# Kernel tuning notes

Measured on AMD Instinct MI355X. Metric: run time of the kernel, lower is better.

Reference implementation:

```python
import jax, jax.numpy as jnp
import numpy as np
import math

B, S, H = 1, 2048, 2048
NH, NKV, HD = 32, 8, 64
GROUPS = NH // NKV
WINDOW = 128
ROPE_THETA = 150000.0
FACTOR = 32.0
ORIG_MAX = 4096.0
BETA_FAST = 32.0
BETA_SLOW = 1.0
SCALE = 1.0 / math.sqrt(HD)


def yarn_rope(q, k, position_ids):
    # q: [B,S,NH,HD], k: [B,S,NKV,HD]
    dim_half = HD // 2
    inv_freq = 1.0 / ROPE_THETA ** (jnp.arange(0, dim_half, 2, dtype=jnp.float32) / dim_half)
    wavelengths = 2.0 * jnp.pi / inv_freq
    ratio = ORIG_MAX / wavelengths
    alpha = jnp.clip((FACTOR * ratio - BETA_FAST) / (BETA_SLOW - BETA_FAST), 0.0, 1.0)
    inv_freq_scaled = inv_freq / FACTOR ** alpha
    freqs = position_ids[:, :, None].astype(jnp.float32) * inv_freq_scaled[None, None, :]
    freqs = jnp.repeat(freqs, 2, axis=-1)  # [B,S,dim_half]
    cos = jnp.cos(freqs)[:, :, None, :]
    sin = jnp.sin(freqs)[:, :, None, :]

    def rotate_half(x):
        # Faithful to source: x already has last dim == dim_half, so x2 is empty
        # and rotate_half(x) == x. Kept literal for exactness.
        x1 = x[..., :dim_half]
        x2 = x[..., dim_half:]
        return jnp.concatenate([-x2, x1], axis=-1)

    q_rot = q[..., :dim_half]
    k_rot = k[..., :dim_half]
    q_rot = q_rot * cos + rotate_half(q_rot) * sin
    k_rot = k_rot * cos + rotate_half(k_rot) * sin
    q = jnp.concatenate([q_rot, q[..., dim_half:]], axis=-1)
    k = jnp.concatenate([k_rot, k[..., dim_half:]], axis=-1)
    return q, k


def setup_inputs() -> dict:
    key = jax.random.key(0)
    ks = jax.random.split(key, 5)
    std = 0.02
    hidden_states = jax.random.normal(ks[0], (B, S, H), dtype=jnp.float32)
    position_ids = jnp.broadcast_to(jnp.arange(S, dtype=jnp.int32)[None, :], (B, S))
    Wq = jax.random.normal(ks[1], (H, NH * HD), dtype=jnp.float32) * std
    Wk = jax.random.normal(ks[2], (H, NKV * HD), dtype=jnp.float32) * std
    Wv = jax.random.normal(ks[3], (H, NKV * HD), dtype=jnp.float32) * std
    Wo = jax.random.normal(ks[4], (NH * HD, H), dtype=jnp.float32) * std
    return {"hidden_states": hidden_states, "position_ids": position_ids,
            "Wq": Wq, "Wk": Wk, "Wv": Wv, "Wo": Wo}


def reference(hidden_states, position_ids, Wq, Wk, Wv, Wo):
    q = (hidden_states @ Wq).reshape(B, S, NH, HD)
    k = (hidden_states @ Wk).reshape(B, S, NKV, HD)
    v = (hidden_states @ Wv).reshape(B, S, NKV, HD)
    q, k = yarn_rope(q, k, position_ids)
    # GQA: repeat kv heads to match query heads
    k = jnp.repeat(k, GROUPS, axis=2)  # [B,S,NH,HD]
    v = jnp.repeat(v, GROUPS, axis=2)
    # scores: [B,NH,S,S]
    scores = jnp.einsum('bqhd,bkhd->bhqk', q, k) * SCALE
    row = jnp.arange(S)[:, None]
    col = jnp.arange(S)[None, :]
    mask = ((jnp.abs(row - col) <= WINDOW) & (row >= col)).astype(jnp.float32)
    scores = scores + (1.0 - mask)[None, None, :, :] * -1e9
    attn = jax.nn.softmax(scores, axis=-1)
    out = jnp.einsum('bhqk,bkhd->bqhd', attn, v).reshape(B, S, NH * HD)
    return out @ Wo
```

## Files before the change

kernel.cpp:

```cpp
#include <hip/hip_runtime.h>

typedef unsigned short u16;
typedef short short8 __attribute__((ext_vector_type(8)));
typedef float f32x4 __attribute__((ext_vector_type(4)));

#define SLEN 2048
#define QKV_LD 3072
#define KOFF 2048
#define VOFF 2560

__device__ __forceinline__ u16 f2b(float f){
  unsigned u = __float_as_uint(f);
  u = u + 0x7FFFu + ((u >> 16) & 1u);
  return (u16)(u >> 16);
}
__device__ __forceinline__ float b2f(u16 v){
  unsigned u = ((unsigned)v) << 16;
  return __uint_as_float(u);
}

__device__ __forceinline__ void gload16(const u16* g, u16* l){
  __builtin_amdgcn_global_load_lds((const __attribute__((address_space(1))) void*)g,
                                   (__attribute__((address_space(3))) void*)l, 16, 0, 0);
}

__global__ __launch_bounds__(256) void k_prep(const float* __restrict__ hidden, u16* __restrict__ hb,
                                              const int* __restrict__ pos, float* __restrict__ g,
                                              const float* __restrict__ Wq, const float* __restrict__ Wk,
                                              const float* __restrict__ Wv, const float* __restrict__ Wo,
                                              u16* __restrict__ Wcat, u16* __restrict__ Wot){
  __shared__ float tile[64][68];
  int b = blockIdx.x, t = threadIdx.x;
  if (b < 4096){
    int i = b * 256 + t;
    float4 v = ((const float4*)hidden)[i];
    ushort4 o;
    o.x = f2b(v.x); o.y = f2b(v.y); o.z = f2b(v.z); o.w = f2b(v.w);
    ((ushort4*)hb)[i] = o;
    return;
  }
  if (b < 4224){
    int idx = (b - 4096) * 256 + t;
    int s = idx >> 4, i = idx & 15;
    float inv = 1.0f / powf(150000.0f, (float)i / 16.0f);
    float wl = 6.283185307179586f / inv;
    float ratio = 4096.0f / wl;
    float alpha = (32.0f * ratio - 32.0f) / (1.0f - 32.0f);
    alpha = fminf(fmaxf(alpha, 0.0f), 1.0f);
    float invs = inv / powf(32.0f, alpha);
    float th = (float)pos[s] * invs;
    double tt = (double)th;
    g[idx] = (float)(cos(tt) + sin(tt));
    return;
  }
  b -= 4224;
  const float* W; u16* D; int Nw, rowoff;
  if (b < 1024)      { W = Wq; D = Wcat; Nw = 2048; rowoff = 0; }
  else if (b < 1280) { W = Wk; D = Wcat; Nw = 512;  rowoff = 2048; b -= 1024; }
  else if (b < 1536) { W = Wv; D = Wcat; Nw = 512;  rowoff = 2560; b -= 1280; }
  else               { W = Wo; D = Wot;  Nw = 2048; rowoff = 0;    b -= 1536; }
  const int kt = b & 31, nt = b >> 5;
  const int k0 = kt * 64, n0 = nt * 64;
  #pragma unroll
  for (int i = 0; i < 4; ++i){
    int slot = i * 256 + t;
    int r = slot >> 4, c4 = (slot & 15) * 4;
    float4 v = *(const float4*)&W[(size_t)(k0 + r) * Nw + n0 + c4];
    tile[r][c4] = v.x; tile[r][c4+1] = v.y; tile[r][c4+2] = v.z; tile[r][c4+3] = v.w;
  }
  __syncthreads();
  #pragma unroll
  for (int i = 0; i < 4; ++i){
    int slot = i * 256 + t;
    int nl = slot >> 4, k4 = (slot & 15) * 4;
    ushort4 o;
    o.x = f2b(tile[k4][nl]);   o.y = f2b(tile[k4+1][nl]);
    o.z = f2b(tile[k4+2][nl]); o.w = f2b(tile[k4+3][nl]);
    *(ushort4*)&D[(size_t)(rowoff + n0 + nl) * 2048 + k0 + k4] = o;
  }
}

template<int OUTF32, int ROPE, int BM, int BN, int MINW>
__global__ __launch_bounds__(256, MINW) void k_gemm(const u16* __restrict__ A, const u16* __restrict__ Bt,
                                                    void* __restrict__ C, const float* __restrict__ g,
                                                    int M, int N, int K){
  constexpr int AG = BM / 32;
  constexpr int BG = BN / 32;
  constexpr int ASZ = BM * 64;
  constexpr int BSZ = BN * 64;
  constexpr int MR = BM / 32;
  constexpr int NR = BN / 32;
  __shared__ __align__(16) u16 Smem[2 * (ASZ + BSZ)];
  const int tid = threadIdx.x;
  const int lane = tid & 63;
  const int w = tid >> 6;
  const int wr = (w >> 1) * (BM / 2);
  const int wc = (w & 1) * (BN / 2);

  const int nbx = M / BM;
  const int nb  = nbx * (N / BN);
  const int q8  = nb >> 3;
  const int bo  = blockIdx.x;
  const int id2 = (bo & 7) * q8 + (bo >> 3);
  const int m0 = (id2 % nbx) * BM;
  const int n0 = (id2 / nbx) * BN;

  const int rl = lane >> 3;
  const int sc = ((lane & 7) ^ rl) << 3;
  const u16* Ag[AG]; const u16* Bg[BG];
  int Ad[AG], Bd[BG];
  #pragma unroll
  for (int i = 0; i < AG; ++i){
    int row0 = w * (AG * 8) + i * 8;
    Ag[i] = A + (size_t)(m0 + row0 + rl) * K + sc;
    Ad[i] = row0 * 64;
  }
  #pragma unroll
  for (int i = 0; i < BG; ++i){
    int row0 = w * (BG * 8) + i * 8;
    Bg[i] = Bt + (size_t)(n0 + row0 + rl) * K + sc;
    Bd[i] = 2 * ASZ + row0 * 64;
  }

  const int fr = lane & 15;
  const int g4 = lane >> 4;

  f32x4 acc[MR][NR] = {};

  auto stage = [&](int buf, int k0){
    #pragma unroll
    for (int i = 0; i < AG; ++i) gload16(Ag[i] + k0, Smem + Ad[i] + buf * ASZ);
    #pragma unroll
    for (int i = 0; i < BG; ++i) gload16(Bg[i] + k0, Smem + Bd[i] + buf * BSZ);
  };

  stage(0, 0);
  int buf = 0;
  const int nt = K >> 6;
  for (int kt = 0; kt < nt; ++kt){
    if (kt + 1 < nt){
      stage(buf ^ 1, (kt + 1) << 6);
      if constexpr (AG + BG == 6)      asm volatile("s_waitcnt vmcnt(6)" ::: "memory");
      else if constexpr (AG + BG == 7) asm volatile("s_waitcnt vmcnt(7)" ::: "memory");
      else                             asm volatile("s_waitcnt vmcnt(8)" ::: "memory");
    } else {
      asm volatile("s_waitcnt vmcnt(0)" ::: "memory");
    }
    __builtin_amdgcn_s_barrier();
    __builtin_amdgcn_sched_barrier(0);
    {
      const u16* Asb = Smem + buf * ASZ;
      const u16* Bsb = Smem + 2 * ASZ + buf * BSZ;
      #pragma unroll
      for (int kk = 0; kk < 2; ++kk){
        const int sw = (((kk * 4 + g4)) ^ (fr & 7)) << 3;
        short8 af[MR], bf[NR];
        #pragma unroll
        for (int m = 0; m < MR; ++m)
          af[m] = *(const short8*)&Asb[(wr + m * 16 + fr) * 64 + sw];
        #pragma unroll
        for (int j = 0; j < NR; ++j)
          bf[j] = *(const short8*)&Bsb[(wc + j * 16 + fr) * 64 + sw];
        #pragma unroll
        for (int m = 0; m < MR; ++m)
          #pragma unroll
          for (int j = 0; j < NR; ++j)
            acc[m][j] = __builtin_amdgcn_mfma_f32_16x16x32_bf16(af[m], bf[j], acc[m][j], 0, 0, 0);
      }
    }
    __builtin_amdgcn_sched_barrier(0);
    __builtin_amdgcn_s_barrier();
    buf ^= 1;
  }

  const int r4 = g4 * 4;
  #pragma unroll
  for (int m = 0; m < MR; ++m)
    #pragma unroll
    for (int j = 0; j < NR; ++j)
      #pragma unroll
      for (int v = 0; v < 4; ++v){
        size_t row = (size_t)(m0 + wr + m * 16 + r4 + v);
        size_t col = (size_t)(n0 + wc + j * 16 + fr);
        float x = acc[m][j][v];
        if (OUTF32){
          ((float*)C)[row * N + col] = x;
        } else {
          if (ROPE){
            int c = (int)col;
            int cj = c & 63;
            if (c < 2560 && cj < 32) x *= g[row * 16 + (cj >> 1)];
            if (c < 2048) x *= 0.125f;
          }
          ((u16*)C)[row * N + col] = f2b(x);
        }
      }
}

#define PST 168
__global__ __launch_bounds__(512, 4) void k_attn(const u16* __restrict__ qkv, u16* __restrict__ aout){
  __shared__ __align__(16) u16 Vt[64 * 264];
  __shared__ __align__(16) u16 P[8 * 16 * PST];
  const int tid = threadIdx.x;
  const int lane = tid & 63;
  const int w = tid >> 6;
  const int id = blockIdx.x;
  const int id2 = (id & 7) * 64 + (id >> 3);
  const int h = id2 >> 4;
  const int q0 = (id2 & 15) * 128;
  const int kvh = h >> 2;
  const int kv0 = q0 - 128;

  {
    const u16* Vg = qkv + VOFF + kvh * 64;
    #pragma unroll
    for (int i = 0; i < 4; ++i){
      int slot = i * 512 + tid;
      int kk = slot >> 3, d8 = (slot & 7) * 8;
      int ks = kv0 + kk; if (ks < 0) ks = 0;
      int ck = kk ^ ((d8 >> 4) << 3);
      short8 v = *(const short8*)(Vg + (size_t)ks * QKV_LD + d8);
      #pragma unroll
      for (int e = 0; e < 8; ++e) Vt[(d8 + e) * 264 + ck] = (u16)v[e];
    }
  }

  const int fr = lane & 15;
  const int kc8 = (lane >> 4) * 8;
  const int r4 = (lane >> 4) * 4;
  const int tt = w >> 2;
  const int wl = w & 3;
  const int nw0 = wl & ~1;
  const int c0 = nw0 * 16;
  const int qt = q0 + tt * 64;
  const int kbase = qt - 128;
  u16* Pw = P + w * 16 * PST;
  const u16* Qg = qkv + h * 64;
  const u16* Kg = qkv + KOFF + kvh * 64;

  short8 qa[2];
  {
    int qrow = qt + wl * 16 + fr;
    qa[0] = *(const short8*)(Qg + (size_t)qrow * QKV_LD + kc8);
    qa[1] = *(const short8*)(Qg + (size_t)qrow * QKV_LD + 32 + kc8);
  }

  f32x4 sc[10];
  __builtin_amdgcn_s_setprio(1);
  #pragma unroll
  for (int n = 0; n < 10; ++n){
    int kr = kbase + (nw0 + n) * 16 + fr;
    int krc = kr < 0 ? 0 : kr;
    short8 kb0 = *(const short8*)(Kg + (size_t)krc * QKV_LD + kc8);
    short8 kb1 = *(const short8*)(Kg + (size_t)krc * QKV_LD + 32 + kc8);
    f32x4 z = {0.f, 0.f, 0.f, 0.f};
    z = __builtin_amdgcn_mfma_f32_16x16x32_bf16(qa[0], kb0, z, 0, 0, 0);
    z = __builtin_amdgcn_mfma_f32_16x16x32_bf16(qa[1], kb1, z, 0, 0, 0);
    sc[n] = z;
  }
  __builtin_amdgcn_s_setprio(0);

  float inv_l[4];
  #pragma unroll
  for (int j = 0; j < 4; ++j){
    int q = qt + wl * 16 + r4 + j;
    float mx = -3.0e38f;
    #pragma unroll
    for (int n = 0; n < 10; ++n){
      int key = kbase + (nw0 + n) * 16 + fr;
      bool valid = (key >= 0) && (key <= q) && (key >= q - 128);
      float s = valid ? sc[n][j] : -1.0e30f;
      sc[n][j] = s;
      mx = fmaxf(mx, s);
    }
    mx = fmaxf(mx, __shfl_xor(mx, 1));
    mx = fmaxf(mx, __shfl_xor(mx, 2));
    mx = fmaxf(mx, __shfl_xor(mx, 4));
    mx = fmaxf(mx, __shfl_xor(mx, 8));
    float sum = 0.f;
    #pragma unroll
    for (int n = 0; n < 10; ++n){
      float pp = exp2f((sc[n][j] - mx) * 1.4426950408889634f);
      sc[n][j] = pp;
      sum += pp;
    }
    sum += __shfl_xor(sum, 1);
    sum += __shfl_xor(sum, 2);
    sum += __shfl_xor(sum, 4);
    sum += __shfl_xor(sum, 8);
    inv_l[j] = 1.0f / sum;
  }

  #pragma unroll
  for (int n = 0; n < 10; ++n)
    #pragma unroll
    for (int j = 0; j < 4; ++j)
      Pw[(r4 + j) * PST + n * 16 + fr] = f2b(sc[n][j]);

  asm volatile("s_waitcnt lgkmcnt(0)" ::: "memory");
  __syncthreads();

  f32x4 ov[4] = {};
  __builtin_amdgcn_s_setprio(1);
  #pragma unroll
  for (int kc = 0; kc < 5; ++kc){
    short8 pa = *(const short8*)&Pw[fr * PST + kc * 32 + kc8];
    #pragma unroll
    for (int f = 0; f < 4; ++f){
      short8 vb = *(const short8*)&Vt[(f * 16 + fr) * 264 + tt * 64 + c0 + kc * 32 + (kc8 ^ (f << 3))];
      ov[f] = __builtin_amdgcn_mfma_f32_16x16x32_bf16(pa, vb, ov[f], 0, 0, 0);
    }
  }
  __builtin_amdgcn_s_setprio(0);

  #pragma unroll
  for (int f = 0; f < 4; ++f)
    #pragma unroll
    for (int j = 0; j < 4; ++j){
      int q = qt + wl * 16 + r4 + j;
      int col = h * 64 + f * 16 + fr;
      aout[(size_t)q * 2048 + col] = f2b(ov[f][j] * inv_l[j]);
    }
}

extern "C" void kernel_launch(void* const* d_in, const int* in_sizes, int n_in,
                              void* d_out, int out_size, void* d_ws, size_t ws_size,
                              hipStream_t stream) {
  const float* hidden = (const float*)d_in[0];
  const int*   pos    = (const int*)d_in[1];
  const float* Wq     = (const float*)d_in[2];
  const float* Wk     = (const float*)d_in[3];
  const float* Wv     = (const float*)d_in[4];
  const float* Wo     = (const float*)d_in[5];
  float* out = (float*)d_out;
  char* ws = (char*)d_ws;

  u16*  hb   = (u16*)(ws);
  u16*  Wcat = (u16*)(ws + ((size_t)8 << 20));
  u16*  Wot  = (u16*)(ws + ((size_t)20 << 20));
  u16*  QKV  = (u16*)(ws + ((size_t)28 << 20));
  float* gtab = (float*)(ws + ((size_t)40 << 20));
  u16*  aout = hb;

  k_prep<<<6784, 256, 0, stream>>>(hidden, hb, pos, gtab, Wq, Wk, Wv, Wo, Wcat, Wot);
  k_gemm<0,1,128,96,2><<<512, 256, 0, stream>>>(hb, Wcat, QKV, gtab, 2048, 3072, 2048);
  k_attn<<<512, 512, 0, stream>>>(QKV, aout);
  k_gemm<1,0,64,128,3><<<512, 256, 0, stream>>>(aout, Wot, out, nullptr, 2048, 2048, 2048);
}
```

Measured before the change: 97.15 us.

## Move Wo transpose into attention tail, triple-buffer output GEMM, fold log2e into Q scale

The Wo fp32-to-bf16 transpose moves out of the prep kernel and into the end of the attention kernel, where each block converts two 64x64 tiles using the freed V LDS buffer. This shrinks the prep launch and fills attention's tail with memory work. The output GEMM switches to three LDS buffers with one barrier per k-step and drops its occupancy hint from 3 to 2. The softmax log2(e) multiply is folded into the Q scale constant, which saves a multiply per score.

```diff
diff --git a/kernel.cpp b/kernel.cpp
--- a/kernel.cpp
+++ b/kernel.cpp
@@ -27,8 +27,8 @@
 __global__ __launch_bounds__(256) void k_prep(const float* __restrict__ hidden, u16* __restrict__ hb,
                                               const int* __restrict__ pos, float* __restrict__ g,
                                               const float* __restrict__ Wq, const float* __restrict__ Wk,
-                                              const float* __restrict__ Wv, const float* __restrict__ Wo,
-                                              u16* __restrict__ Wcat, u16* __restrict__ Wot){
+                                              const float* __restrict__ Wv,
+                                              u16* __restrict__ Wcat){
   __shared__ float tile[64][68];
   int b = blockIdx.x, t = threadIdx.x;
   if (b < 4096){
@@ -54,11 +54,10 @@
     return;
   }
   b -= 4224;
-  const float* W; u16* D; int Nw, rowoff;
-  if (b < 1024)      { W = Wq; D = Wcat; Nw = 2048; rowoff = 0; }
-  else if (b < 1280) { W = Wk; D = Wcat; Nw = 512;  rowoff = 2048; b -= 1024; }
-  else if (b < 1536) { W = Wv; D = Wcat; Nw = 512;  rowoff = 2560; b -= 1280; }
-  else               { W = Wo; D = Wot;  Nw = 2048; rowoff = 0;    b -= 1536; }
+  const float* W; int Nw, rowoff;
+  if (b < 1024)      { W = Wq; Nw = 2048; rowoff = 0; }
+  else if (b < 1280) { W = Wk; Nw = 512;  rowoff = 2048; b -= 1024; }
+  else               { W = Wv; Nw = 512;  rowoff = 2560; b -= 1280; }
   const int kt = b & 31, nt = b >> 5;
   const int k0 = kt * 64, n0 = nt * 64;
   #pragma unroll
@@ -76,11 +75,11 @@
     ushort4 o;
     o.x = f2b(tile[k4][nl]);   o.y = f2b(tile[k4+1][nl]);
     o.z = f2b(tile[k4+2][nl]); o.w = f2b(tile[k4+3][nl]);
-    *(ushort4*)&D[(size_t)(rowoff + n0 + nl) * 2048 + k0 + k4] = o;
-  }
-}
-
-template<int OUTF32, int ROPE, int BM, int BN, int MINW>
+    *(ushort4*)&Wcat[(size_t)(rowoff + n0 + nl) * 2048 + k0 + k4] = o;
+  }
+}
+
+template<int OUTF32, int ROPE, int BM, int BN, int MINW, int NBUF>
 __global__ __launch_bounds__(256, MINW) void k_gemm(const u16* __restrict__ A, const u16* __restrict__ Bt,
                                                     void* __restrict__ C, const float* __restrict__ g,
                                                     int M, int N, int K){
@@ -90,7 +89,7 @@
   constexpr int BSZ = BN * 64;
   constexpr int MR = BM / 32;
   constexpr int NR = BN / 32;
-  __shared__ __align__(16) u16 Smem[2 * (ASZ + BSZ)];
+  __shared__ __align__(16) u16 Smem[NBUF * (ASZ + BSZ)];
   const int tid = threadIdx.x;
   const int lane = tid & 63;
   const int w = tid >> 6;
@@ -119,7 +118,7 @@
   for (int i = 0; i < BG; ++i){
     int row0 = w * (BG * 8) + i * 8;
     Bg[i] = Bt + (size_t)(n0 + row0 + rl) * K + sc;
-    Bd[i] = 2 * ASZ + row0 * 64;
+    Bd[i] = NBUF * ASZ + row0 * 64;
   }
 
   const int fr = lane & 15;
@@ -138,8 +137,9 @@
   int buf = 0;
   const int nt = K >> 6;
   for (int kt = 0; kt < nt; ++kt){
+    int nxt = (buf + 1 == NBUF) ? 0 : buf + 1;
     if (kt + 1 < nt){
-      stage(buf ^ 1, (kt + 1) << 6);
+      stage(nxt, (kt + 1) << 6);
       if constexpr (AG + BG == 6)      asm volatile("s_waitcnt vmcnt(6)" ::: "memory");
       else if constexpr (AG + BG == 7) asm volatile("s_waitcnt vmcnt(7)" ::: "memory");
       else                             asm volatile("s_waitcnt vmcnt(8)" ::: "memory");
@@ -150,7 +150,7 @@
     __builtin_amdgcn_sched_barrier(0);
     {
       const u16* Asb = Smem + buf * ASZ;
-      const u16* Bsb = Smem + 2 * ASZ + buf * BSZ;
+      const u16* Bsb = Smem + NBUF * ASZ + buf * BSZ;
       #pragma unroll
       for (int kk = 0; kk < 2; ++kk){
         const int sw = (((kk * 4 + g4)) ^ (fr & 7)) << 3;
@@ -168,9 +168,11 @@
             acc[m][j] = __builtin_amdgcn_mfma_f32_16x16x32_bf16(af[m], bf[j], acc[m][j], 0, 0, 0);
       }
     }
-    __builtin_amdgcn_sched_barrier(0);
-    __builtin_amdgcn_s_barrier();
-    buf ^= 1;
+    if constexpr (NBUF == 2){
+      __builtin_amdgcn_sched_barrier(0);
+      __builtin_amdgcn_s_barrier();
+    }
+    buf = nxt;
   }
 
   const int r4 = g4 * 4;
@@ -190,7 +192,7 @@
             int c = (int)col;
             int cj = c & 63;
             if (c < 2560 && cj < 32) x *= g[row * 16 + (cj >> 1)];
-            if (c < 2048) x *= 0.125f;
+            if (c < 2048) x *= 0.18033688f;
           }
           ((u16*)C)[row * N + col] = f2b(x);
         }
@@ -198,7 +200,8 @@
 }
 
 #define PST 168
-__global__ __launch_bounds__(512, 4) void k_attn(const u16* __restrict__ qkv, u16* __restrict__ aout){
+__global__ __launch_bounds__(512, 4) void k_attn(const u16* __restrict__ qkv, u16* __restrict__ aout,
+                                                 const float* __restrict__ Wo, u16* __restrict__ Wot){
   __shared__ __align__(16) u16 Vt[64 * 264];
   __shared__ __align__(16) u16 P[8 * 16 * PST];
   const int tid = threadIdx.x;
@@ -280,7 +283,7 @@
     float sum = 0.f;
     #pragma unroll
     for (int n = 0; n < 10; ++n){
-      float pp = exp2f((sc[n][j] - mx) * 1.4426950408889634f);
+      float pp = exp2f(sc[n][j] - mx);
       sc[n][j] = pp;
       sum += pp;
     }
@@ -321,6 +324,33 @@
       int col = h * 64 + f * 16 + fr;
       aout[(size_t)q * 2048 + col] = f2b(ov[f][j] * inv_l[j]);
     }
+
+  __syncthreads();
+  float (*tf)[68] = (float(*)[68])Vt;
+  #pragma unroll
+  for (int tix = 0; tix < 2; ++tix){
+    int tile = id * 2 + tix;
+    int kt2 = tile & 31, nt2 = tile >> 5;
+    int k0 = kt2 * 64, n0 = nt2 * 64;
+    #pragma unroll
+    for (int i = 0; i < 2; ++i){
+      int slot = i * 512 + tid;
+      int r = slot >> 4, c4 = (slot & 15) * 4;
+      float4 v = *(const float4*)&Wo[(size_t)(k0 + r) * 2048 + n0 + c4];
+      tf[r][c4] = v.x; tf[r][c4+1] = v.y; tf[r][c4+2] = v.z; tf[r][c4+3] = v.w;
+    }
+    __syncthreads();
+    #pragma unroll
+    for (int i = 0; i < 2; ++i){
+      int slot = i * 512 + tid;
+      int nl = slot >> 4, k4 = (slot & 15) * 4;
+      ushort4 o;
+      o.x = f2b(tf[k4][nl]);   o.y = f2b(tf[k4+1][nl]);
+      o.z = f2b(tf[k4+2][nl]); o.w = f2b(tf[k4+3][nl]);
+      *(ushort4*)&Wot[(size_t)(n0 + nl) * 2048 + k0 + k4] = o;
+    }
+    __syncthreads();
+  }
 }
 
 extern "C" void kernel_launch(void* const* d_in, const int* in_sizes, int n_in,
@@ -342,8 +372,8 @@
   float* gtab = (float*)(ws + ((size_t)40 << 20));
   u16*  aout = hb;
 
-  k_prep<<<6784, 256, 0, stream>>>(hidden, hb, pos, gtab, Wq, Wk, Wv, Wo, Wcat, Wot);
-  k_gemm<0,1,128,96,2><<<512, 256, 0, stream>>>(hb, Wcat, QKV, gtab, 2048, 3072, 2048);
-  k_attn<<<512, 512, 0, stream>>>(QKV, aout);
-  k_gemm<1,0,64,128,3><<<512, 256, 0, stream>>>(aout, Wot, out, nullptr, 2048, 2048, 2048);
-}
+  k_prep<<<5760, 256, 0, stream>>>(hidden, hb, pos, gtab, Wq, Wk, Wv, Wcat);
+  k_gemm<0,1,128,96,2,2><<<512, 256, 0, stream>>>(hb, Wcat, QKV, gtab, 2048, 3072, 2048);
+  k_attn<<<512, 512, 0, stream>>>(QKV, aout, Wo, Wot);
+  k_gemm<1,0,64,128,2,3><<<512, 256, 0, stream>>>(aout, Wot, out, nullptr, 2048, 2048, 2048);
+}
```

Measured after the change: 94.65 us. -2.6%, faster.
